# Performance work log

Hardware: AMD Instinct MI355X
Metric: run time of the kernel (lower is better)

Reference implementation:

```python
import jax, jax.numpy as jnp
import numpy as np

B, T_Q, T_K, H = 16, 1024, 1024, 1024


def _linear_params(key, fan_in, fan_out):
    kw, kb = jax.random.split(key)
    bound = 1.0 / np.sqrt(fan_in)
    W = jax.random.uniform(kw, (fan_out, fan_in), jnp.float32, -bound, bound)
    b = jax.random.uniform(kb, (fan_out,), jnp.float32, -bound, bound)
    return W, b


def setup_inputs() -> dict:
    key = jax.random.key(0)
    ks = jax.random.split(key, 6)
    query = jax.random.normal(ks[0], (B, T_Q, H), jnp.float32)
    keys = jax.random.normal(ks[1], (B, T_K, H), jnp.float32)
    values = jax.random.normal(ks[2], (B, T_K, H), jnp.float32)
    Wq, bq = _linear_params(ks[3], H, H)
    Wk, bk = _linear_params(ks[4], H, H)
    Wo, bo = _linear_params(ks[5], H, H)
    return {"query": query, "keys": keys, "values": values,
            "Wq": Wq, "bq": bq, "Wk": Wk, "bk": bk, "Wo": Wo, "bo": bo}


def reference(query, keys, values, Wq, bq, Wk, bk, Wo, bo):
    # Linear projections (torch Linear: x @ W.T + b)
    q = jnp.einsum('bth,oh->bto', query, Wq) + bq   # (B, T_Q, H)
    k = jnp.einsum('bsh,oh->bso', keys, Wk) + bk    # (B, T_K, H)
    # Unscaled scores -> softmax over key axis (dropout is identity at eval)
    scores = jnp.einsum('bto,bso->bts', q, k)       # (B, T_Q, T_K)
    attn = jax.nn.softmax(scores, axis=-1)
    ctx = jnp.einsum('bts,bsh->bth', attn, values)  # note: raw values, value_fc unused in source
    ctx = ctx / jnp.sqrt(jnp.float32(values.shape[1]))
    out = jnp.einsum('bth,oh->bto', ctx, Wo) + bo
    return out
```

## Files before the change

kernel.cpp:

```cpp
#include <hip/hip_runtime.h>
#include <math.h>

typedef __attribute__((ext_vector_type(4))) float f32x4;
typedef __attribute__((ext_vector_type(8))) _Float16 h16x8;
typedef __attribute__((ext_vector_type(4))) short s16x4;

__device__ inline unsigned short f2h(float f) {
    union { _Float16 h; unsigned short u; } v; v.h = (_Float16)f; return v.u;
}
__device__ inline float h2f(unsigned short u) {
    union { unsigned short u; _Float16 h; } v; v.u = u; return (float)v.h;
}

__device__ inline void async16(const void* g, void* l) {
    __builtin_amdgcn_global_load_lds(
        (const __attribute__((address_space(1))) unsigned int*)g,
        (__attribute__((address_space(3))) unsigned int*)l, 16, 0, 0);
}

#define BM 256
#define BN 256
#define BK 64
#define NTHREADS 512


__device__ inline void stage_half(const unsigned short* g, int row0, int kel, int K,
                                  unsigned ldsbase, char* smem, int tid) {
    const int rl  = tid >> 3;
    const int scb = ((tid & 7) ^ (rl & 7)) << 4;
    char* wb = smem + ldsbase + (unsigned)((tid >> 6) << 10);
#pragma unroll
    for (int s = 0; s < 2; ++s) {
        long off = ((long)(row0 + s * 64 + rl) * K + kel) * 2 + scb;
        async16((const char*)g + off, wb + s * 8192);
    }
}

__device__ inline h16x8 ld_frag(const char* smem, unsigned base, int row, int kbyte) {
    unsigned off = base + (unsigned)(row * 128) + (unsigned)(kbyte ^ ((row & 7) << 4));
    return *(const h16x8*)(smem + off);
}

__device__ inline void xcd_swizzle(int& bx, int& by, int& bz) {
    const long gx = gridDim.x, gy = gridDim.y;
    const long nwg = gx * gy * (long)gridDim.z;
    const long hw  = ((long)blockIdx.z * gy + blockIdx.y) * gx + blockIdx.x;
    const long qq = nwg >> 3, rr = nwg & 7;
    const long xcd = hw & 7, pos = hw >> 3;
    const long lg = (xcd < rr) ? xcd * (qq + 1) + pos
                               : rr * (qq + 1) + (xcd - rr) * qq + pos;
    bx = (int)(lg % gx);
    const long rem = lg / gx;
    by = (int)(rem % gy);
    bz = (int)(rem / gy);
}

template<int OM>
__global__ __launch_bounds__(NTHREADS, 2)
void gemm256(const unsigned short* __restrict__ A,
             const unsigned short* __restrict__ B,
             const float* __restrict__ bias,
             void* __restrict__ C, int N, int K,
             long sA, long sB, long sC, float scale)
{
    __shared__ __align__(16) char smem[131072];

    const int tid  = threadIdx.x;
    const int wv   = tid >> 6;
    const int lane = tid & 63;
    const int wr = wv >> 2, wc = wv & 3;
    const int lrow = lane & 15;
    const int kq16 = (lane >> 4) * 16;

    int bx, by, bz; xcd_swizzle(bx, by, bz);
    const int n0 = bx * BN;
    const int m0 = by * BM;

    const unsigned short* Ag = A + (long)bz * sA;
    const unsigned short* Bg = B + (long)bz * sB;
    const int NT = K / BK;

    auto stageA = [&](int t, int h) {
        stage_half(Ag, m0 + h * 128, t * BK, K,
                   (unsigned)(((t & 1) << 16) + (h << 14)), smem, tid);
    };
    auto stageB = [&](int t, int h) {
        stage_half(Bg, n0 + h * 128, t * BK, K,
                   (unsigned)(((t & 1) << 16) + 32768 + (h << 14)), smem, tid);
    };

    f32x4 acc[8][4];
#pragma unroll
    for (int i = 0; i < 8; ++i)
#pragma unroll
        for (int j = 0; j < 4; ++j) acc[i][j] = (f32x4){0.f, 0.f, 0.f, 0.f};

    const unsigned AbaseW = (unsigned)(wr * 16384);
    const unsigned BbaseW = (unsigned)(32768 + (wc >> 1) * 16384);
    const int brow0 = (wc & 1) * 64;

    stageB(0, 0); stageB(0, 1); stageA(0, 0); stageA(0, 1); stageB(1, 0); stageB(1, 1);
    asm volatile("s_waitcnt vmcnt(4)" ::: "memory");
    __builtin_amdgcn_s_barrier();

    h16x8 bfr[4][2], afr[2][2];

    for (int i = 0; i < NT / 2; ++i) {
        const int t1 = 2 * i + 1, t2 = 2 * i + 2, t3 = 2 * i + 3;
#pragma unroll
        for (int half = 0; half < 2; ++half) {
            const unsigned hb = half ? 65536u : 0u;
#pragma unroll
            for (int q = 0; q < 4; ++q) {
                if (q == 0) {
#pragma unroll
                    for (int j = 0; j < 4; ++j)
#pragma unroll
                        for (int ks = 0; ks < 2; ++ks)
                            bfr[j][ks] = ld_frag(smem, hb + BbaseW, brow0 + j * 16 + lrow, ks * 64 + kq16);
                }
#pragma unroll
                for (int f = 0; f < 2; ++f)
#pragma unroll
                    for (int ks = 0; ks < 2; ++ks)
                        afr[f][ks] = ld_frag(smem, hb + AbaseW, q * 32 + f * 16 + lrow, ks * 64 + kq16);
                if (half == 0) {
                    if (q == 0)      stageA(t1, 0);
                    else if (q == 1) stageA(t1, 1);
                    else if (q == 2) { if (t2 < NT) stageB(t2, 0); }
                    else             { if (t2 < NT) stageB(t2, 1); }
                } else {
                    if (q == 0)      { if (t2 < NT) stageA(t2, 0); }
                    else if (q == 1) { if (t2 < NT) stageA(t2, 1); }
                    else if (q == 2) { if (t3 < NT) stageB(t3, 0); }
                    else             { if (t3 < NT) stageB(t3, 1); }
                }

                __builtin_amdgcn_s_barrier();
                asm volatile("s_waitcnt lgkmcnt(0)" ::: "memory");
                __builtin_amdgcn_sched_barrier(0);
                __builtin_amdgcn_s_setprio(1);
#pragma unroll
                for (int ks = 0; ks < 2; ++ks)
#pragma unroll
                    for (int f = 0; f < 2; ++f)
#pragma unroll
                        for (int j = 0; j < 4; ++j)
                            acc[2 * q + f][j] = __builtin_amdgcn_mfma_f32_16x16x32_f16(
                                afr[f][ks], bfr[j][ks], acc[2 * q + f][j], 0, 0, 0);
                __builtin_amdgcn_s_setprio(0);
                if (q == 3) {
                    const int tn = half ? t3 : t2;
                    if (tn < NT) { asm volatile("s_waitcnt vmcnt(4)" ::: "memory"); }
                    else         { asm volatile("s_waitcnt vmcnt(0)" ::: "memory"); }
                }
                __builtin_amdgcn_s_barrier();
            }
        }
    }

#pragma unroll
    for (int j = 0; j < 4; ++j) {
        const int col = n0 + wc * 64 + j * 16 + lrow;
        const float bb = bias ? bias[col] : 0.f;
#pragma unroll
        for (int mi = 0; mi < 8; ++mi) {
#pragma unroll
            for (int r = 0; r < 4; ++r) {
                const long row = m0 + wr * 128 + mi * 16 + (lane >> 4) * 4 + r;
                const float v = acc[mi][j][r] * scale + bb;
                const long idx = (long)bz * sC + row * (long)N + col;
                if constexpr (OM == 0) ((float*)C)[idx] = v;
                else                   ((unsigned short*)C)[idx] = f2h(v);
            }
        }
    }
}

__global__ __launch_bounds__(256)
void conv_f16(const float* __restrict__ in, unsigned short* __restrict__ out, int n)
{
    int i = (blockIdx.x * 256 + threadIdx.x) * 4;
    if (i >= n) return;
    float4 v = *(const float4*)(in + i);
    s16x4 o = {(short)f2h(v.x), (short)f2h(v.y), (short)f2h(v.z), (short)f2h(v.w)};
    *(s16x4*)(out + i) = o;
}

__global__ __launch_bounds__(256)
void transpose_f16(const float* __restrict__ in, unsigned short* __restrict__ out)
{
    __shared__ float tile[32][33];
    const long base = (long)blockIdx.z * 1024 * 1024;
    const int h0 = blockIdx.x * 32, t0 = blockIdx.y * 32;
    for (int i = threadIdx.y; i < 32; i += 8)
        tile[i][threadIdx.x] = in[base + (long)(t0 + i) * 1024 + h0 + threadIdx.x];
    __syncthreads();
    for (int i = threadIdx.y; i < 32; i += 8)
        out[base + (long)(h0 + i) * 1024 + t0 + threadIdx.x] = f2h(tile[threadIdx.x][i]);
}

__global__ __launch_bounds__(256)
void softmax_ip(unsigned short* __restrict__ S)
{
    long row = blockIdx.x;
    const int tid = threadIdx.x;
    s16x4 raw = *(s16x4*)(S + row * 1024 + tid * 4);
    float v0 = h2f((unsigned short)raw[0]), v1 = h2f((unsigned short)raw[1]);
    float v2 = h2f((unsigned short)raw[2]), v3 = h2f((unsigned short)raw[3]);
    float m = fmaxf(fmaxf(v0, v1), fmaxf(v2, v3));
#pragma unroll
    for (int off = 1; off < 64; off <<= 1) m = fmaxf(m, __shfl_xor(m, off));
    __shared__ float redm[4];
    int wave = tid >> 6, lane = tid & 63;
    if (lane == 0) redm[wave] = m;
    __syncthreads();
    m = fmaxf(fmaxf(redm[0], redm[1]), fmaxf(redm[2], redm[3]));

    float e0 = expf(v0 - m), e1 = expf(v1 - m), e2 = expf(v2 - m), e3 = expf(v3 - m);
    float s = e0 + e1 + e2 + e3;
#pragma unroll
    for (int off = 1; off < 64; off <<= 1) s += __shfl_xor(s, off);
    __shared__ float reds[4];
    if (lane == 0) reds[wave] = s;
    __syncthreads();
    s = reds[0] + reds[1] + reds[2] + reds[3];
    float inv = 1.f / s;
    s16x4 o = {(short)f2h(e0 * inv), (short)f2h(e1 * inv),
               (short)f2h(e2 * inv), (short)f2h(e3 * inv)};
    *(s16x4*)(S + row * 1024 + tid * 4) = o;
}

extern "C" void kernel_launch(void* const* d_in, const int* in_sizes, int n_in,
                              void* d_out, int out_size, void* d_ws, size_t ws_size,
                              hipStream_t stream)
{
    const float* query  = (const float*)d_in[0];
    const float* keys   = (const float*)d_in[1];
    const float* values = (const float*)d_in[2];
    const float* Wq     = (const float*)d_in[3];
    const float* bq     = (const float*)d_in[4];
    const float* Wk     = (const float*)d_in[5];
    const float* bk     = (const float*)d_in[6];
    const float* Wo     = (const float*)d_in[7];
    const float* bo     = (const float*)d_in[8];

    const int  T = 1024, H = 1024;
    const long NE = 16384L * 1024;
    const long NW = 1024L * 1024;

    size_t need = (size_t)(NE * 5 + NW * 3) * sizeof(unsigned short);
    if (ws_size < need) return;

    unsigned short* ws  = (unsigned short*)d_ws;
    unsigned short* Xq  = ws;
    unsigned short* Xk  = Xq + NE;
    unsigned short* qf  = Xk + NE;
    unsigned short* kf  = qf + NE;
    unsigned short* vT  = kf + NE;
    unsigned short* Wqh = vT + NE;
    unsigned short* Wkh = Wqh + NW;
    unsigned short* Woh = Wkh + NW;
    unsigned short* sc  = Xq;
    unsigned short* ctx = Xk;

    conv_f16<<<16384, 256, 0, stream>>>(query, Xq, (int)NE);
    conv_f16<<<16384, 256, 0, stream>>>(keys,  Xk, (int)NE);
    conv_f16<<<1024,  256, 0, stream>>>(Wq, Wqh, (int)NW);
    conv_f16<<<1024,  256, 0, stream>>>(Wk, Wkh, (int)NW);
    conv_f16<<<1024,  256, 0, stream>>>(Wo, Woh, (int)NW);
    transpose_f16<<<dim3(32, 32, 16), dim3(32, 8), 0, stream>>>(values, vT);

    gemm256<1><<<dim3(4, 64, 1), NTHREADS, 0, stream>>>(
        Xq, Wqh, bq, qf, H, H, 0, 0, 0, 1.f);
    gemm256<1><<<dim3(4, 64, 1), NTHREADS, 0, stream>>>(
        Xk, Wkh, bk, kf, H, H, 0, 0, 0, 1.f);
    gemm256<1><<<dim3(4, 4, 16), NTHREADS, 0, stream>>>(
        qf, kf, nullptr, sc, T, H, (long)T * H, (long)T * H, (long)T * T, 1.f);
    softmax_ip<<<16384, 256, 0, stream>>>(sc);
    gemm256<1><<<dim3(4, 4, 16), NTHREADS, 0, stream>>>(
        sc, vT, nullptr, ctx, H, T, (long)T * T, (long)T * H, (long)T * H, 1.f / 32.f);
    gemm256<0><<<dim3(4, 64, 1), NTHREADS, 0, stream>>>(
        ctx, Woh, bo, d_out, H, H, 0, 0, 0, 1.f);
}
```

Measured before the change: 312.7 us.

## Fold Wq and Wk into a single H×H matrix to drop the K projection

```diff
diff --git a/kernel.cpp b/kernel.cpp
--- a/kernel.cpp
+++ b/kernel.cpp
@@ -3,6 +3,7 @@
 
 typedef __attribute__((ext_vector_type(4))) float f32x4;
 typedef __attribute__((ext_vector_type(8))) _Float16 h16x8;
+typedef __attribute__((ext_vector_type(8))) short s16x8;
 typedef __attribute__((ext_vector_type(4))) short s16x4;
 
 __device__ inline unsigned short f2h(float f) {
@@ -24,14 +25,14 @@
 #define NTHREADS 512
 
 
-__device__ inline void stage_half(const unsigned short* g, int row0, int kel, int K,
+__device__ inline void stage_half(const unsigned short* g, int row0, int kel, int pitch,
                                   unsigned ldsbase, char* smem, int tid) {
     const int rl  = tid >> 3;
     const int scb = ((tid & 7) ^ (rl & 7)) << 4;
     char* wb = smem + ldsbase + (unsigned)((tid >> 6) << 10);
 #pragma unroll
     for (int s = 0; s < 2; ++s) {
-        long off = ((long)(row0 + s * 64 + rl) * K + kel) * 2 + scb;
+        long off = ((long)(row0 + s * 64 + rl) * pitch + kel) * 2 + scb;
         async16((const char*)g + off, wb + s * 8192);
     }
 }
@@ -60,8 +61,8 @@
 void gemm256(const unsigned short* __restrict__ A,
              const unsigned short* __restrict__ B,
              const float* __restrict__ bias,
-             void* __restrict__ C, int N, int K,
-             long sA, long sB, long sC, float scale)
+             void* __restrict__ C, int N, int lenK, int pitch,
+             long sA, long sB, long sC, long sBias, float scale)
 {
     __shared__ __align__(16) char smem[131072];
 
@@ -78,14 +79,14 @@
 
     const unsigned short* Ag = A + (long)bz * sA;
     const unsigned short* Bg = B + (long)bz * sB;
-    const int NT = K / BK;
+    const int NT = lenK / BK;
 
     auto stageA = [&](int t, int h) {
-        stage_half(Ag, m0 + h * 128, t * BK, K,
+        stage_half(Ag, m0 + h * 128, t * BK, pitch,
                    (unsigned)(((t & 1) << 16) + (h << 14)), smem, tid);
     };
     auto stageB = [&](int t, int h) {
-        stage_half(Bg, n0 + h * 128, t * BK, K,
+        stage_half(Bg, n0 + h * 128, t * BK, pitch,
                    (unsigned)(((t & 1) << 16) + 32768 + (h << 14)), smem, tid);
     };
 
@@ -162,7 +163,7 @@
 #pragma unroll
     for (int j = 0; j < 4; ++j) {
         const int col = n0 + wc * 64 + j * 16 + lrow;
-        const float bb = bias ? bias[col] : 0.f;
+        const float bb = bias ? bias[(long)bz * sBias + col] : 0.f;
 #pragma unroll
         for (int mi = 0; mi < 8; ++mi) {
 #pragma unroll
@@ -201,6 +202,56 @@
 }
 
 __global__ __launch_bounds__(256)
+void w2_kernel(const float* __restrict__ Wk, const float* __restrict__ bq,
+               float* __restrict__ w2)
+{
+    __shared__ float part[4][64];
+    const int tx = threadIdx.x & 63;
+    const int ty = threadIdx.x >> 6;
+    const int h  = blockIdx.x * 64 + tx;
+    float s = 0.f;
+    for (int o = ty * 256; o < ty * 256 + 256; ++o)
+        s = fmaf(Wk[(long)o * 1024 + h], bq[o], s);
+    part[ty][tx] = s;
+    __syncthreads();
+    if (ty == 0) w2[h] = part[0][tx] + part[1][tx] + part[2][tx] + part[3][tx];
+}
+
+__global__ __launch_bounds__(256)
+void matvec_v(const unsigned short* __restrict__ Xk, const float* __restrict__ w2,
+              float* __restrict__ v)
+{
+    const int wave = threadIdx.x >> 6, lane = threadIdx.x & 63;
+    const long row = (long)blockIdx.x * 4 + wave;
+    const unsigned short* p = Xk + row * 1024 + lane * 16;
+    float s = 0.f;
+#pragma unroll
+    for (int c = 0; c < 2; ++c) {
+        s16x8 hv = *(const s16x8*)(p + c * 8);
+#pragma unroll
+        for (int e = 0; e < 8; ++e)
+            s = fmaf(h2f((unsigned short)hv[e]), w2[lane * 16 + c * 8 + e], s);
+    }
+#pragma unroll
+    for (int off = 1; off < 64; off <<= 1) s += __shfl_xor(s, off);
+    if (lane == 0) v[row] = s;
+}
+
+__global__ __launch_bounds__(256)
+void reduce4(const float* __restrict__ p, unsigned short* __restrict__ MT)
+{
+    const long i = ((long)blockIdx.x * 256 + threadIdx.x) * 4;
+    const long S = 1024L * 1024;
+    float4 a = *(const float4*)(p + i);
+    float4 b = *(const float4*)(p + S + i);
+    float4 c = *(const float4*)(p + 2 * S + i);
+    float4 d = *(const float4*)(p + 3 * S + i);
+    s16x4 o = {(short)f2h(a.x + b.x + c.x + d.x), (short)f2h(a.y + b.y + c.y + d.y),
+               (short)f2h(a.z + b.z + c.z + d.z), (short)f2h(a.w + b.w + c.w + d.w)};
+    *(s16x4*)(MT + i) = o;
+}
+
+__global__ __launch_bounds__(256)
 void softmax_ip(unsigned short* __restrict__ S)
 {
     long row = blockIdx.x;
@@ -244,42 +295,57 @@
     const float* bk     = (const float*)d_in[6];
     const float* Wo     = (const float*)d_in[7];
     const float* bo     = (const float*)d_in[8];
+    (void)bk;
 
     const int  T = 1024, H = 1024;
     const long NE = 16384L * 1024;
     const long NW = 1024L * 1024;
 
-    size_t need = (size_t)(NE * 5 + NW * 3) * sizeof(unsigned short);
+    size_t need = (size_t)(NE * 4 + NW * 12 + 40960) * sizeof(unsigned short);
     if (ws_size < need) return;
 
-    unsigned short* ws  = (unsigned short*)d_ws;
-    unsigned short* Xq  = ws;
-    unsigned short* Xk  = Xq + NE;
-    unsigned short* qf  = Xk + NE;
-    unsigned short* kf  = qf + NE;
-    unsigned short* vT  = kf + NE;
-    unsigned short* Wqh = vT + NE;
-    unsigned short* Wkh = Wqh + NW;
-    unsigned short* Woh = Wkh + NW;
-    unsigned short* sc  = Xq;
-    unsigned short* ctx = Xk;
+    unsigned short* ws   = (unsigned short*)d_ws;
+    unsigned short* Xq   = ws;
+    unsigned short* Xk   = Xq + NE;
+    unsigned short* vT   = Xk + NE;
+    unsigned short* P1   = vT + NE;
+    unsigned short* WqT  = P1 + NE;
+    unsigned short* WkT  = WqT + NW;
+    unsigned short* Woh  = WkT + NW;
+    unsigned short* MT   = Woh + NW;
+    float*          part = (float*)(MT + NW);
+    float*          w2   = (float*)(MT + NW * 9);
+    float*          vvec = w2 + 1024;
+    unsigned short* sc   = Xq;
+    unsigned short* ctx  = P1;
 
     conv_f16<<<16384, 256, 0, stream>>>(query, Xq, (int)NE);
     conv_f16<<<16384, 256, 0, stream>>>(keys,  Xk, (int)NE);
-    conv_f16<<<1024,  256, 0, stream>>>(Wq, Wqh, (int)NW);
-    conv_f16<<<1024,  256, 0, stream>>>(Wk, Wkh, (int)NW);
-    conv_f16<<<1024,  256, 0, stream>>>(Wo, Woh, (int)NW);
+    transpose_f16<<<dim3(32, 32, 1), dim3(32, 8), 0, stream>>>(Wq, WqT);
+    transpose_f16<<<dim3(32, 32, 1), dim3(32, 8), 0, stream>>>(Wk, WkT);
+    conv_f16<<<1024, 256, 0, stream>>>(Wo, Woh, (int)NW);
     transpose_f16<<<dim3(32, 32, 16), dim3(32, 8), 0, stream>>>(values, vT);
+    w2_kernel<<<16, 256, 0, stream>>>(Wk, bq, w2);
+
+    gemm256<0><<<dim3(4, 4, 4), NTHREADS, 0, stream>>>(
+        WkT, WqT, nullptr, part, 1024, 256, 1024, 256, 256, (long)NW, 0, 1.f);
+    reduce4<<<1024, 256, 0, stream>>>(part, MT);
 
     gemm256<1><<<dim3(4, 64, 1), NTHREADS, 0, stream>>>(
-        Xq, Wqh, bq, qf, H, H, 0, 0, 0, 1.f);
-    gemm256<1><<<dim3(4, 64, 1), NTHREADS, 0, stream>>>(
-        Xk, Wkh, bk, kf, H, H, 0, 0, 0, 1.f);
+        Xq, MT, nullptr, P1, H, H, H, 0, 0, 0, 0, 1.f);
+
+    matvec_v<<<4096, 256, 0, stream>>>(Xk, w2, vvec);
+
     gemm256<1><<<dim3(4, 4, 16), NTHREADS, 0, stream>>>(
-        qf, kf, nullptr, sc, T, H, (long)T * H, (long)T * H, (long)T * T, 1.f);
+        P1, Xk, vvec, sc, T, H, H,
+        (long)T * H, (long)T * H, (long)T * T, (long)T, 1.f);
+
     softmax_ip<<<16384, 256, 0, stream>>>(sc);
+
     gemm256<1><<<dim3(4, 4, 16), NTHREADS, 0, stream>>>(
-        sc, vT, nullptr, ctx, H, T, (long)T * T, (long)T * H, (long)T * H, 1.f / 32.f);
+        sc, vT, nullptr, ctx, H, T, T,
+        (long)T * T, (long)T * H, (long)T * H, 0, 1.f / 32.f);
+
     gemm256<0><<<dim3(4, 64, 1), NTHREADS, 0, stream>>>(
-        ctx, Woh, bo, d_out, H, H, 0, 0, 0, 1.f);
-}
+        ctx, Woh, bo, d_out, H, H, H, 0, 0, 0, 0, 1.f);
+}
```

After: 306.6 us. About the same (-2.0%).
